# Kernel optimization log

Hardware: AMD Instinct MI355X
Metric: run time of the kernel (lower is better)

The kernel has to match this reference:

```python
import jax, jax.numpy as jnp
import numpy as np

WBIT = 8
ABIT = 8
NESTBIT = 4
SHIFTBIT = WBIT - NESTBIT  # 4
OUT, IN, TOKENS = 8192, 8192, 256


def setup_inputs() -> dict:
    key = jax.random.key(0)
    ks = jax.random.split(key, 6)
    x = jax.random.normal(ks[0], (TOKENS, IN), dtype=jnp.float32)
    # two 4-bit high-group values packed per byte along in_features
    packed_high = jax.random.randint(ks[1], (OUT, IN // 2), 0, 256, dtype=jnp.int32)
    # 5-bit low-group values (offset-16 signed), one per byte
    packed_low = jax.random.randint(ks[2], (OUT, IN), 0, 32, dtype=jnp.int32)
    scale = jax.random.uniform(ks[3], (OUT, 1), dtype=jnp.float32) * 0.01 + 1e-4
    zero_point = jax.random.normal(ks[4], (OUT, 1), dtype=jnp.float32)
    bias = jax.random.normal(ks[5], (OUT,), dtype=jnp.float32)
    act_scale = jnp.ones((), dtype=jnp.float32) * 0.05
    return {"x": x, "packed_high": packed_high, "packed_low": packed_low,
            "scale": scale, "zero_point": zero_point, "bias": bias,
            "act_scale": act_scale}


def _quant_input(x, s):
    # abit symmetric fake-quant with straight-through estimator
    n = 2 ** (ABIT - 1)
    xq = jnp.clip(jnp.round(x / s), -n, n - 1) * s
    return x + jax.lax.stop_gradient(xq - x)


def _dequant_weight(packed_high, packed_low, scale, zero_point):
    # unpack two 4-bit nibbles per byte -> signed [-8, 7]
    hi = (packed_high >> 4) & 0xF
    lo = packed_high & 0xF
    qh = jnp.stack([hi, lo], axis=-1).reshape(packed_high.shape[0], -1) - 8  # [OUT, IN]
    ql = packed_low - 16  # 5-bit signed [-16, 15]
    n = 2 ** (WBIT - 1)
    q = jnp.clip(qh * (2 ** SHIFTBIT) + ql, -n, n - 1)
    # linear_dequantize; torch wraps this in no_grad -> weight is a constant
    w = (q.astype(jnp.float32) - zero_point) * scale
    return jax.lax.stop_gradient(w)


def reference(x, packed_high, packed_low, scale, zero_point, bias, act_scale):
    xq = _quant_input(x, act_scale)
    w = _dequant_weight(packed_high, packed_low, scale, zero_point)  # [OUT, IN]
    return jnp.dot(xq, w.T) + bias  # [TOKENS, OUT]
```

## Files before the change

### kernel.cpp

```cpp
#include <hip/hip_runtime.h>


typedef int v4i __attribute__((ext_vector_type(4)));

#define TOKENS 256
#define INF 8192
#define OUTF 8192

__global__ __launch_bounds__(256) void quant_x_kernel(
    const float* __restrict__ x, const float* __restrict__ act_scale,
    signed char* __restrict__ xi8, int* __restrict__ rowsum)
{
    const int t = blockIdx.x;
    const int j = threadIdx.x;
    const float s = act_scale[0];
    const float4* xrow = (const float4*)(x + (size_t)t * INF);
    int* qrow = (int*)(xi8 + (size_t)t * INF);
    int lsum = 0;
#pragma unroll
    for (int c = 0; c < 8; ++c) {
        float4 v = xrow[j + c * 256];
        int q0 = (int)rintf(v.x / s); q0 = q0 < -128 ? -128 : (q0 > 127 ? 127 : q0);
        int q1 = (int)rintf(v.y / s); q1 = q1 < -128 ? -128 : (q1 > 127 ? 127 : q1);
        int q2 = (int)rintf(v.z / s); q2 = q2 < -128 ? -128 : (q2 > 127 ? 127 : q2);
        int q3 = (int)rintf(v.w / s); q3 = q3 < -128 ? -128 : (q3 > 127 ? 127 : q3);
        qrow[j + c * 256] = (q0 & 255) | ((q1 & 255) << 8) | ((q2 & 255) << 16) | ((q3 & 255) << 24);
        lsum += q0 + q1 + q2 + q3;
    }
#pragma unroll
    for (int off = 32; off > 0; off >>= 1) lsum += __shfl_down(lsum, off, 64);
    __shared__ int wsum[4];
    if ((j & 63) == 0) wsum[j >> 6] = lsum;
    __syncthreads();
    if (j == 0) rowsum[t] = wsum[0] + wsum[1] + wsum[2] + wsum[3];
}

__global__ __launch_bounds__(512) void gemm_kernel(
    const signed char* __restrict__ xi8, const int* __restrict__ rowsum,
    const int* __restrict__ packed_high, const int* __restrict__ packed_low,
    const float* __restrict__ scale, const float* __restrict__ zero_point,
    const float* __restrict__ bias, const float* __restrict__ act_scale,
    float* __restrict__ out)
{
    __shared__ __align__(16) signed char Blds[2][4][32][16];

    const int tid  = threadIdx.x;
    const int lane = tid & 63;
    const int w    = tid >> 6;
    const int n0   = blockIdx.x * 32;

    const int so = tid >> 4;
    const int si = (tid & 15) << 2;
    const int* pl_ptr = packed_low  + (size_t)(n0 + so) * INF       + si;
    const int* ph_ptr = packed_high + (size_t)(n0 + so) * (INF / 2) + (si >> 1);

    const signed char* a_ptr = xi8 + (size_t)((w << 5) + (lane & 15)) * INF + ((lane >> 4) << 4);

    v4i acc00 = {0, 0, 0, 0}, acc01 = {0, 0, 0, 0}, acc10 = {0, 0, 0, 0}, acc11 = {0, 0, 0, 0};

    int4 pl = *(const int4*)pl_ptr;
    int2 ph = *(const int2*)ph_ptr;
    v4i  a0 = *(const v4i*)a_ptr;
    v4i  a1 = *(const v4i*)(a_ptr + 16 * INF);

#define PROCESS_TILE(T)                                                                   \
    {                                                                                     \
                                           \
        int q0 = (ph.x & 0xF0)        + pl.x - 144; if (q0 < -128) q0 = -128;             \
        int q1 = ((ph.x & 0x0F) << 4) + pl.y - 144; if (q1 < -128) q1 = -128;             \
        int q2 = (ph.y & 0xF0)        + pl.z - 144; if (q2 < -128) q2 = -128;             \
        int q3 = ((ph.y & 0x0F) << 4) + pl.w - 144; if (q3 < -128) q3 = -128;             \
        int packed = (q0 & 255) | ((q1 & 255) << 8) | ((q2 & 255) << 16) | ((q3 & 255) << 24); \
        *(int*)&Blds[(T) & 1][si >> 4][so][si & 12] = packed;                             \
              \
              \
        asm volatile("s_waitcnt lgkmcnt(0)" ::: "memory");                                \
        __builtin_amdgcn_s_barrier();                                                     \
        v4i b0 = *(const v4i*)&Blds[(T) & 1][lane >> 4][lane & 15][0];                    \
        v4i b1 = *(const v4i*)&Blds[(T) & 1][lane >> 4][16 + (lane & 15)][0];             \
        acc00 = __builtin_amdgcn_mfma_i32_16x16x64_i8(a0, b0, acc00, 0, 0, 0);            \
        acc01 = __builtin_amdgcn_mfma_i32_16x16x64_i8(a0, b1, acc01, 0, 0, 0);            \
        acc10 = __builtin_amdgcn_mfma_i32_16x16x64_i8(a1, b0, acc10, 0, 0, 0);            \
        acc11 = __builtin_amdgcn_mfma_i32_16x16x64_i8(a1, b1, acc11, 0, 0, 0);            \
    }

    for (int t = 0; t < 127; ++t) {
        const int koff = (t + 1) << 6;
        int4 pl_n = *(const int4*)(pl_ptr + koff);
        int2 ph_n = *(const int2*)(ph_ptr + (koff >> 1));
        v4i  a0_n = *(const v4i*)(a_ptr + koff);
        v4i  a1_n = *(const v4i*)(a_ptr + 16 * INF + koff);
        PROCESS_TILE(t);
        pl = pl_n; ph = ph_n; a0 = a0_n; a1 = a1_n;
    }
    PROCESS_TILE(127);
#undef PROCESS_TILE

    const float as  = act_scale[0];
    const int col   = lane & 15;
    const int rbase = (w << 5) + ((lane >> 4) << 2);

#define EPILOGUE(ACC, MI, CI)                                                  \
    {                                                                          \
        const int o   = n0 + (CI) * 16 + col;                                  \
        const float sc = as * scale[o];                                        \
        const float zo = zero_point[o];                                        \
        const float bo = bias[o];                                              \
        _Pragma("unroll")                                                      \
        for (int r = 0; r < 4; ++r) {                                          \
            const int trow = rbase + (MI) * 16 + r;                            \
            const float f = (float)ACC[r] - zo * (float)rowsum[trow];          \
            out[(size_t)trow * OUTF + o] = sc * f + bo;                        \
        }                                                                      \
    }
    EPILOGUE(acc00, 0, 0)
    EPILOGUE(acc01, 0, 1)
    EPILOGUE(acc10, 1, 0)
    EPILOGUE(acc11, 1, 1)
#undef EPILOGUE
}

extern "C" void kernel_launch(void* const* d_in, const int* in_sizes, int n_in,
                              void* d_out, int out_size, void* d_ws, size_t ws_size,
                              hipStream_t stream)
{
    const float* x           = (const float*)d_in[0];
    const int*   packed_high = (const int*)d_in[1];
    const int*   packed_low  = (const int*)d_in[2];
    const float* scale       = (const float*)d_in[3];
    const float* zero_point  = (const float*)d_in[4];
    const float* bias        = (const float*)d_in[5];
    const float* act_scale   = (const float*)d_in[6];
    float* out = (float*)d_out;

    signed char* xi8 = (signed char*)d_ws;
    int* rowsum = (int*)((char*)d_ws + (size_t)TOKENS * INF);

    quant_x_kernel<<<TOKENS, 256, 0, stream>>>(x, act_scale, xi8, rowsum);
    gemm_kernel<<<OUTF / 32, 512, 0, stream>>>(xi8, rowsum, packed_high, packed_low,
                                               scale, zero_point, bias, act_scale, out);
}
```

Baseline: 496.4 us.

## Retile int8 GEMM to 16-column blocks with 2-stage prefetch and padded LDS

Switches the dequant-GEMM to 16 output columns per block with 256 threads, where each wave covers 64 tokens and each iteration handles K=128 with two MFMAs per A/B pair. Weight loads are nontemporal, and both A and B tiles are register-prefetched two iterations ahead using ping-pong register sets. LDS rows are padded (stride 288) so writes and reads hit fewer bank conflicts. The goal is fewer barriers per K, more blocks for occupancy, and better latency hiding for the streamed packed weights. The cost is more registers and more A re-reads from L2 across twice as many blocks.

Result: slower. 512.6 us (+3.3%).

```diff
diff --git a/kernel.cpp b/kernel.cpp
--- a/kernel.cpp
+++ b/kernel.cpp
@@ -2,10 +2,14 @@
 
 
 typedef int v4i __attribute__((ext_vector_type(4)));
+typedef int v2i __attribute__((ext_vector_type(2)));
 
 #define TOKENS 256
 #define INF 8192
 #define OUTF 8192
+#define BN 16
+#define KSTEP 128
+#define NITER 64
 
 __global__ __launch_bounds__(256) void quant_x_kernel(
     const float* __restrict__ x, const float* __restrict__ act_scale,
@@ -35,89 +39,110 @@
     if (j == 0) rowsum[t] = wsum[0] + wsum[1] + wsum[2] + wsum[3];
 }
 
-__global__ __launch_bounds__(512) void gemm_kernel(
+__device__ __forceinline__ int unpack4(v4i pl, v2i ph) {
+    int q0 = (ph[0] & 0xF0)        + pl[0] - 144; q0 = q0 < -128 ? -128 : q0;
+    int q1 = ((ph[0] & 0x0F) << 4) + pl[1] - 144; q1 = q1 < -128 ? -128 : q1;
+    int q2 = (ph[1] & 0xF0)        + pl[2] - 144; q2 = q2 < -128 ? -128 : q2;
+    int q3 = ((ph[1] & 0x0F) << 4) + pl[3] - 144; q3 = q3 < -128 ? -128 : q3;
+    return (q0 & 255) | ((q1 & 255) << 8) | ((q2 & 255) << 16) | ((q3 & 255) << 24);
+}
+
+__global__ __launch_bounds__(256, 2) void gemm_kernel(
     const signed char* __restrict__ xi8, const int* __restrict__ rowsum,
     const int* __restrict__ packed_high, const int* __restrict__ packed_low,
     const float* __restrict__ scale, const float* __restrict__ zero_point,
     const float* __restrict__ bias, const float* __restrict__ act_scale,
     float* __restrict__ out)
 {
-    __shared__ __align__(16) signed char Blds[2][4][32][16];
+    __shared__ __align__(16) char Blds[2 * 2304];
 
     const int tid  = threadIdx.x;
     const int lane = tid & 63;
     const int w    = tid >> 6;
-    const int n0   = blockIdx.x * 32;
+    const int n0   = blockIdx.x * BN;
 
     const int so = tid >> 4;
     const int si = (tid & 15) << 2;
     const int* pl_ptr = packed_low  + (size_t)(n0 + so) * INF       + si;
     const int* ph_ptr = packed_high + (size_t)(n0 + so) * (INF / 2) + (si >> 1);
+    const int wof0 = (si >> 4) * 288 + so * 16 + (si & 12);
+    const int wof1 = wof0 + 4 * 288;
 
-    const signed char* a_ptr = xi8 + (size_t)((w << 5) + (lane & 15)) * INF + ((lane >> 4) << 4);
+    const int rof0 = (lane >> 4) * 288 + (lane & 15) * 16;
+    const int rof1 = rof0 + 4 * 288;
 
-    v4i acc00 = {0, 0, 0, 0}, acc01 = {0, 0, 0, 0}, acc10 = {0, 0, 0, 0}, acc11 = {0, 0, 0, 0};
+    const signed char* aptr = xi8 + (size_t)((w << 6) + (lane & 15)) * INF + ((lane >> 4) << 4);
 
-    int4 pl = *(const int4*)pl_ptr;
-    int2 ph = *(const int2*)ph_ptr;
-    v4i  a0 = *(const v4i*)a_ptr;
-    v4i  a1 = *(const v4i*)(a_ptr + 16 * INF);
+    v4i acc0 = {0,0,0,0}, acc1 = {0,0,0,0}, acc2 = {0,0,0,0}, acc3 = {0,0,0,0};
 
-#define PROCESS_TILE(T)                                                                   \
-    {                                                                                     \
-                                           \
-        int q0 = (ph.x & 0xF0)        + pl.x - 144; if (q0 < -128) q0 = -128;             \
-        int q1 = ((ph.x & 0x0F) << 4) + pl.y - 144; if (q1 < -128) q1 = -128;             \
-        int q2 = (ph.y & 0xF0)        + pl.z - 144; if (q2 < -128) q2 = -128;             \
-        int q3 = ((ph.y & 0x0F) << 4) + pl.w - 144; if (q3 < -128) q3 = -128;             \
-        int packed = (q0 & 255) | ((q1 & 255) << 8) | ((q2 & 255) << 16) | ((q3 & 255) << 24); \
-        *(int*)&Blds[(T) & 1][si >> 4][so][si & 12] = packed;                             \
-              \
-              \
-        asm volatile("s_waitcnt lgkmcnt(0)" ::: "memory");                                \
-        __builtin_amdgcn_s_barrier();                                                     \
-        v4i b0 = *(const v4i*)&Blds[(T) & 1][lane >> 4][lane & 15][0];                    \
-        v4i b1 = *(const v4i*)&Blds[(T) & 1][lane >> 4][16 + (lane & 15)][0];             \
-        acc00 = __builtin_amdgcn_mfma_i32_16x16x64_i8(a0, b0, acc00, 0, 0, 0);            \
-        acc01 = __builtin_amdgcn_mfma_i32_16x16x64_i8(a0, b1, acc01, 0, 0, 0);            \
-        acc10 = __builtin_amdgcn_mfma_i32_16x16x64_i8(a1, b0, acc10, 0, 0, 0);            \
-        acc11 = __builtin_amdgcn_mfma_i32_16x16x64_i8(a1, b1, acc11, 0, 0, 0);            \
+    v4i plA0, plA1, plB0, plB1;
+    v2i phA0, phA1, phB0, phB1;
+    v4i aA[8], aB[8];
+
+#define LOAD_B(PL0, PL1, PH0, PH1, T) {                                         \
+        const int k0_ = (T) * KSTEP;                                            \
+        PL0 = __builtin_nontemporal_load((const v4i*)(pl_ptr + k0_));           \
+        PL1 = __builtin_nontemporal_load((const v4i*)(pl_ptr + k0_ + 64));      \
+        PH0 = __builtin_nontemporal_load((const v2i*)(ph_ptr + (k0_ >> 1)));    \
+        PH1 = __builtin_nontemporal_load((const v2i*)(ph_ptr + (k0_ >> 1) + 32)); }
+
+#define LOAD_A(AR, T) {                                                         \
+        const int k0_ = (T) * KSTEP;                                            \
+        _Pragma("unroll")                                                       \
+        for (int f = 0; f < 4; ++f) {                                           \
+            AR[f]     = *(const v4i*)(aptr + f * 16 * INF + k0_);               \
+            AR[f + 4] = *(const v4i*)(aptr + f * 16 * INF + k0_ + 64);          \
+        } }
+
+#define BODY(PL0, PL1, PH0, PH1, AR, T, BUF) {                                  \
+        *(int*)(Blds + (BUF) * 2304 + wof0) = unpack4(PL0, PH0);                \
+        *(int*)(Blds + (BUF) * 2304 + wof1) = unpack4(PL1, PH1);                \
+        { const int tn_ = ((T) + 2 < NITER) ? (T) + 2 : NITER - 1;              \
+          LOAD_B(PL0, PL1, PH0, PH1, tn_); }                                    \
+             \
+             \
+        asm volatile("s_waitcnt lgkmcnt(0)" ::: "memory");                      \
+        __builtin_amdgcn_s_barrier();                                           \
+        v4i b0_ = *(const v4i*)(Blds + (BUF) * 2304 + rof0);                    \
+        v4i b1_ = *(const v4i*)(Blds + (BUF) * 2304 + rof1);                    \
+        acc0 = __builtin_amdgcn_mfma_i32_16x16x64_i8(AR[0], b0_, acc0, 0, 0, 0);\
+        acc1 = __builtin_amdgcn_mfma_i32_16x16x64_i8(AR[1], b0_, acc1, 0, 0, 0);\
+        acc2 = __builtin_amdgcn_mfma_i32_16x16x64_i8(AR[2], b0_, acc2, 0, 0, 0);\
+        acc3 = __builtin_amdgcn_mfma_i32_16x16x64_i8(AR[3], b0_, acc3, 0, 0, 0);\
+        acc0 = __builtin_amdgcn_mfma_i32_16x16x64_i8(AR[4], b1_, acc0, 0, 0, 0);\
+        acc1 = __builtin_amdgcn_mfma_i32_16x16x64_i8(AR[5], b1_, acc1, 0, 0, 0);\
+        acc2 = __builtin_amdgcn_mfma_i32_16x16x64_i8(AR[6], b1_, acc2, 0, 0, 0);\
+        acc3 = __builtin_amdgcn_mfma_i32_16x16x64_i8(AR[7], b1_, acc3, 0, 0, 0);\
+        { const int tn_ = ((T) + 2 < NITER) ? (T) + 2 : NITER - 1;              \
+          LOAD_A(AR, tn_); } }
+
+    LOAD_B(plA0, plA1, phA0, phA1, 0); LOAD_A(aA, 0);
+    LOAD_B(plB0, plB1, phB0, phB1, 1); LOAD_A(aB, 1);
+
+    for (int t = 0; t < NITER; t += 2) {
+        BODY(plA0, plA1, phA0, phA1, aA, t,     0);
+        BODY(plB0, plB1, phB0, phB1, aB, t + 1, 1);
     }
+#undef BODY
+#undef LOAD_A
+#undef LOAD_B
 
-    for (int t = 0; t < 127; ++t) {
-        const int koff = (t + 1) << 6;
-        int4 pl_n = *(const int4*)(pl_ptr + koff);
-        int2 ph_n = *(const int2*)(ph_ptr + (koff >> 1));
-        v4i  a0_n = *(const v4i*)(a_ptr + koff);
-        v4i  a1_n = *(const v4i*)(a_ptr + 16 * INF + koff);
-        PROCESS_TILE(t);
-        pl = pl_n; ph = ph_n; a0 = a0_n; a1 = a1_n;
-    }
-    PROCESS_TILE(127);
-#undef PROCESS_TILE
+    const float as = act_scale[0];
+    const int col  = lane & 15;
+    const int o    = n0 + col;
+    const float sc = as * scale[o];
+    const float zo = zero_point[o];
+    const float bo = bias[o];
+    const int rbase = (w << 6) + ((lane >> 4) << 2);
 
-    const float as  = act_scale[0];
-    const int col   = lane & 15;
-    const int rbase = (w << 5) + ((lane >> 4) << 2);
-
-#define EPILOGUE(ACC, MI, CI)                                                  \
-    {                                                                          \
-        const int o   = n0 + (CI) * 16 + col;                                  \
-        const float sc = as * scale[o];                                        \
-        const float zo = zero_point[o];                                        \
-        const float bo = bias[o];                                              \
-        _Pragma("unroll")                                                      \
-        for (int r = 0; r < 4; ++r) {                                          \
-            const int trow = rbase + (MI) * 16 + r;                            \
-            const float f = (float)ACC[r] - zo * (float)rowsum[trow];          \
-            out[(size_t)trow * OUTF + o] = sc * f + bo;                        \
-        }                                                                      \
-    }
-    EPILOGUE(acc00, 0, 0)
-    EPILOGUE(acc01, 0, 1)
-    EPILOGUE(acc10, 1, 0)
-    EPILOGUE(acc11, 1, 1)
-#undef EPILOGUE
+#define EPI(ACC, F) { _Pragma("unroll")                                        \
+    for (int r = 0; r < 4; ++r) {                                              \
+        const int trow = rbase + (F) * 16 + r;                                 \
+        const float fv = (float)ACC[r] - zo * (float)rowsum[trow];             \
+        out[(size_t)trow * OUTF + o] = fmaf(sc, fv, bo);                       \
+    } }
+    EPI(acc0, 0) EPI(acc1, 1) EPI(acc2, 2) EPI(acc3, 3)
+#undef EPI
 }
 
 extern "C" void kernel_launch(void* const* d_in, const int* in_sizes, int n_in,
@@ -137,6 +162,6 @@
     int* rowsum = (int*)((char*)d_ws + (size_t)TOKENS * INF);
 
     quant_x_kernel<<<TOKENS, 256, 0, stream>>>(x, act_scale, xi8, rowsum);
-    gemm_kernel<<<OUTF / 32, 512, 0, stream>>>(xi8, rowsum, packed_high, packed_low,
+    gemm_kernel<<<OUTF / BN, 256, 0, stream>>>(xi8, rowsum, packed_high, packed_low,
                                                scale, zero_point, bias, act_scale, out);
 }
```

## Split K across waves with MFMA-ready activation layout and LDS reduction

Applied to the files above, without the earlier changes.

The quantize kernel now writes int8 activations in a fragment-ordered layout, so each lane's 16-byte A operand for a 64-wide K block is one contiguous load. The GEMM moves to 16 output columns per block with 4 waves that split K. Each wave covers all 256 tokens with 16 accumulators, so every dequantized weight fragment is reused across the whole token dimension. The per-tile LDS barrier for sharing weights is gone, and partial sums are combined with LDS atomics before the epilogue. In exchange it uses heavy registers (16 A fragments plus 16 accumulators), reloads activations per block, and adds a cross-wave atomic reduction.

Measured after the change: 492.8 us. About the same (-0.7%).

```diff
diff --git a/kernel.cpp b/kernel.cpp
--- a/kernel.cpp
+++ b/kernel.cpp
@@ -6,25 +6,33 @@
 #define TOKENS 256
 #define INF 8192
 #define OUTF 8192
+#define NSTEP 32
 
 __global__ __launch_bounds__(256) void quant_x_kernel(
     const float* __restrict__ x, const float* __restrict__ act_scale,
-    signed char* __restrict__ xi8, int* __restrict__ rowsum)
+    int* __restrict__ apk, int* __restrict__ rowsum)
 {
     const int t = blockIdx.x;
     const int j = threadIdx.x;
     const float s = act_scale[0];
     const float4* xrow = (const float4*)(x + (size_t)t * INF);
-    int* qrow = (int*)(xi8 + (size_t)t * INF);
+    const int f    = t >> 4;
+    const int llow = t & 15;
     int lsum = 0;
 #pragma unroll
     for (int c = 0; c < 8; ++c) {
-        float4 v = xrow[j + c * 256];
+        const int kw = j + c * 256;
+        float4 v = xrow[kw];
         int q0 = (int)rintf(v.x / s); q0 = q0 < -128 ? -128 : (q0 > 127 ? 127 : q0);
         int q1 = (int)rintf(v.y / s); q1 = q1 < -128 ? -128 : (q1 > 127 ? 127 : q1);
         int q2 = (int)rintf(v.z / s); q2 = q2 < -128 ? -128 : (q2 > 127 ? 127 : q2);
         int q3 = (int)rintf(v.w / s); q3 = q3 < -128 ? -128 : (q3 > 127 ? 127 : q3);
-        qrow[j + c * 256] = (q0 & 255) | ((q1 & 255) << 8) | ((q2 & 255) << 16) | ((q3 & 255) << 24);
+        const int word = (q0 & 255) | ((q1 & 255) << 8) | ((q2 & 255) << 16) | ((q3 & 255) << 24);
+        const int k0 = kw << 2;
+        const int kb = k0 >> 6;
+        const int ks = k0 & 63;
+        const int lane = ((ks >> 4) << 4) + llow;
+        apk[kb * 4096 + f * 256 + (lane << 2) + ((ks & 15) >> 2)] = word;
         lsum += q0 + q1 + q2 + q3;
     }
 #pragma unroll
@@ -35,89 +43,94 @@
     if (j == 0) rowsum[t] = wsum[0] + wsum[1] + wsum[2] + wsum[3];
 }
 
-__global__ __launch_bounds__(512) void gemm_kernel(
-    const signed char* __restrict__ xi8, const int* __restrict__ rowsum,
+__device__ __forceinline__ int unpack4(v4i pl, int pha, int phb) {
+    int q0 = (pha & 0xF0)        + pl[0] - 144; q0 = q0 < -128 ? -128 : q0;
+    int q1 = ((pha & 0x0F) << 4) + pl[1] - 144; q1 = q1 < -128 ? -128 : q1;
+    int q2 = (phb & 0xF0)        + pl[2] - 144; q2 = q2 < -128 ? -128 : q2;
+    int q3 = ((phb & 0x0F) << 4) + pl[3] - 144; q3 = q3 < -128 ? -128 : q3;
+    return (q0 & 255) | ((q1 & 255) << 8) | ((q2 & 255) << 16) | ((q3 & 255) << 24);
+}
+
+__global__ __launch_bounds__(256) void gemm_kernel(
+    const int* __restrict__ apk, const int* __restrict__ rowsum,
     const int* __restrict__ packed_high, const int* __restrict__ packed_low,
     const float* __restrict__ scale, const float* __restrict__ zero_point,
     const float* __restrict__ bias, const float* __restrict__ act_scale,
     float* __restrict__ out)
 {
-    __shared__ __align__(16) signed char Blds[2][4][32][16];
+    __shared__ int accbuf[16][4][64];
 
     const int tid  = threadIdx.x;
     const int lane = tid & 63;
     const int w    = tid >> 6;
-    const int n0   = blockIdx.x * 32;
+    const int n0   = blockIdx.x * 16;
+    const int col  = lane & 15;
+    const int kq16 = lane >> 4;
 
-    const int so = tid >> 4;
-    const int si = (tid & 15) << 2;
-    const int* pl_ptr = packed_low  + (size_t)(n0 + so) * INF       + si;
-    const int* ph_ptr = packed_high + (size_t)(n0 + so) * (INF / 2) + (si >> 1);
+    const int o     = n0 + col;
+    const int kbase = w * (NSTEP * 64) + kq16 * 16;
+    const int* pl = packed_low  + (size_t)o * INF       + kbase;
+    const int* ph = packed_high + (size_t)o * (INF / 2) + (kbase >> 1);
 
-    const signed char* a_ptr = xi8 + (size_t)((w << 5) + (lane & 15)) * INF + ((lane >> 4) << 4);
+    const int* ab = apk + w * NSTEP * 4096 + (lane << 2);
 
-    v4i acc00 = {0, 0, 0, 0}, acc01 = {0, 0, 0, 0}, acc10 = {0, 0, 0, 0}, acc11 = {0, 0, 0, 0};
+    v4i acc[16];
+#pragma unroll
+    for (int f = 0; f < 16; ++f) acc[f] = (v4i){0, 0, 0, 0};
 
-    int4 pl = *(const int4*)pl_ptr;
-    int2 ph = *(const int2*)ph_ptr;
-    v4i  a0 = *(const v4i*)a_ptr;
-    v4i  a1 = *(const v4i*)(a_ptr + 16 * INF);
+    v4i a[16], plv[4], phv[2];
+#pragma unroll
+    for (int m = 0; m < 4; ++m) plv[m] = *(const v4i*)(pl + 4 * m);
+#pragma unroll
+    for (int m = 0; m < 2; ++m) phv[m] = *(const v4i*)(ph + 4 * m);
+#pragma unroll
+    for (int f = 0; f < 16; ++f) a[f] = *(const v4i*)(ab + f * 256);
 
-#define PROCESS_TILE(T)                                                                   \
-    {                                                                                     \
-                                           \
-        int q0 = (ph.x & 0xF0)        + pl.x - 144; if (q0 < -128) q0 = -128;             \
-        int q1 = ((ph.x & 0x0F) << 4) + pl.y - 144; if (q1 < -128) q1 = -128;             \
-        int q2 = (ph.y & 0xF0)        + pl.z - 144; if (q2 < -128) q2 = -128;             \
-        int q3 = ((ph.y & 0x0F) << 4) + pl.w - 144; if (q3 < -128) q3 = -128;             \
-        int packed = (q0 & 255) | ((q1 & 255) << 8) | ((q2 & 255) << 16) | ((q3 & 255) << 24); \
-        *(int*)&Blds[(T) & 1][si >> 4][so][si & 12] = packed;                             \
-              \
-              \
-        asm volatile("s_waitcnt lgkmcnt(0)" ::: "memory");                                \
-        __builtin_amdgcn_s_barrier();                                                     \
-        v4i b0 = *(const v4i*)&Blds[(T) & 1][lane >> 4][lane & 15][0];                    \
-        v4i b1 = *(const v4i*)&Blds[(T) & 1][lane >> 4][16 + (lane & 15)][0];             \
-        acc00 = __builtin_amdgcn_mfma_i32_16x16x64_i8(a0, b0, acc00, 0, 0, 0);            \
-        acc01 = __builtin_amdgcn_mfma_i32_16x16x64_i8(a0, b1, acc01, 0, 0, 0);            \
-        acc10 = __builtin_amdgcn_mfma_i32_16x16x64_i8(a1, b0, acc10, 0, 0, 0);            \
-        acc11 = __builtin_amdgcn_mfma_i32_16x16x64_i8(a1, b1, acc11, 0, 0, 0);            \
+    for (int t = 0; t < NSTEP; ++t) {
+        const int tn = (t + 1) & (NSTEP - 1);
+        v4i b;
+        b[0] = unpack4(plv[0], phv[0][0], phv[0][1]);
+        b[1] = unpack4(plv[1], phv[0][2], phv[0][3]);
+        b[2] = unpack4(plv[2], phv[1][0], phv[1][1]);
+        b[3] = unpack4(plv[3], phv[1][2], phv[1][3]);
+#pragma unroll
+        for (int m = 0; m < 4; ++m) plv[m] = *(const v4i*)(pl + tn * 64 + 4 * m);
+#pragma unroll
+        for (int m = 0; m < 2; ++m) phv[m] = *(const v4i*)(ph + tn * 32 + 4 * m);
+        const int* abn = ab + tn * 4096;
+#pragma unroll
+        for (int f = 0; f < 16; ++f) {
+            acc[f] = __builtin_amdgcn_mfma_i32_16x16x64_i8(a[f], b, acc[f], 0, 0, 0);
+            a[f] = *(const v4i*)(abn + f * 256);
+        }
     }
 
-    for (int t = 0; t < 127; ++t) {
-        const int koff = (t + 1) << 6;
-        int4 pl_n = *(const int4*)(pl_ptr + koff);
-        int2 ph_n = *(const int2*)(ph_ptr + (koff >> 1));
-        v4i  a0_n = *(const v4i*)(a_ptr + koff);
-        v4i  a1_n = *(const v4i*)(a_ptr + 16 * INF + koff);
-        PROCESS_TILE(t);
-        pl = pl_n; ph = ph_n; a0 = a0_n; a1 = a1_n;
+    int* flat = &accbuf[0][0][0];
+#pragma unroll
+    for (int i = 0; i < 4; ++i) *(v4i*)(flat + tid * 16 + i * 4) = (v4i){0, 0, 0, 0};
+    __syncthreads();
+#pragma unroll
+    for (int f = 0; f < 16; ++f)
+#pragma unroll
+        for (int r = 0; r < 4; ++r)
+            atomicAdd(&accbuf[f][r][lane], acc[f][r]);
+    __syncthreads();
+
+    const float as = act_scale[0];
+    const float sc = as * scale[o];
+    const float zo = zero_point[o];
+    const float bo = bias[o];
+#pragma unroll
+    for (int ff = 0; ff < 4; ++ff) {
+        const int f = (w << 2) + ff;
+        const int rbase = f * 16 + kq16 * 4;
+        v4i rs = *(const v4i*)(rowsum + rbase);
+#pragma unroll
+        for (int r = 0; r < 4; ++r) {
+            const float fv = (float)accbuf[f][r][lane] - zo * (float)rs[r];
+            out[(size_t)(rbase + r) * OUTF + o] = fmaf(sc, fv, bo);
+        }
     }
-    PROCESS_TILE(127);
-#undef PROCESS_TILE
-
-    const float as  = act_scale[0];
-    const int col   = lane & 15;
-    const int rbase = (w << 5) + ((lane >> 4) << 2);
-
-#define EPILOGUE(ACC, MI, CI)                                                  \
-    {                                                                          \
-        const int o   = n0 + (CI) * 16 + col;                                  \
-        const float sc = as * scale[o];                                        \
-        const float zo = zero_point[o];                                        \
-        const float bo = bias[o];                                              \
-        _Pragma("unroll")                                                      \
-        for (int r = 0; r < 4; ++r) {                                          \
-            const int trow = rbase + (MI) * 16 + r;                            \
-            const float f = (float)ACC[r] - zo * (float)rowsum[trow];          \
-            out[(size_t)trow * OUTF + o] = sc * f + bo;                        \
-        }                                                                      \
-    }
-    EPILOGUE(acc00, 0, 0)
-    EPILOGUE(acc01, 0, 1)
-    EPILOGUE(acc10, 1, 0)
-    EPILOGUE(acc11, 1, 1)
-#undef EPILOGUE
 }
 
 extern "C" void kernel_launch(void* const* d_in, const int* in_sizes, int n_in,
@@ -133,10 +146,10 @@
     const float* act_scale   = (const float*)d_in[6];
     float* out = (float*)d_out;
 
-    signed char* xi8 = (signed char*)d_ws;
+    int* apk    = (int*)d_ws;
     int* rowsum = (int*)((char*)d_ws + (size_t)TOKENS * INF);
 
-    quant_x_kernel<<<TOKENS, 256, 0, stream>>>(x, act_scale, xi8, rowsum);
-    gemm_kernel<<<OUTF / 32, 512, 0, stream>>>(xi8, rowsum, packed_high, packed_low,
+    quant_x_kernel<<<TOKENS, 256, 0, stream>>>(x, act_scale, apk, rowsum);
+    gemm_kernel<<<OUTF / 16, 256, 0, stream>>>(apk, rowsum, packed_high, packed_low,
                                                scale, zero_point, bias, act_scale, out);
 }
```
